# Kernel optimization log

Hardware: AMD Instinct MI355X
Metric: run time of the kernel (lower is better)

The kernel has to match this reference:

```python
import jax, jax.numpy as jnp
import numpy as np

H_IMG, W_IMG = 224, 224  # image_size default in forward


def setup_inputs() -> dict:
    key = jax.random.key(0)
    k0, k1, k2 = jax.random.split(key, 3)
    B, C, M, N = 4, 256, 1024, 16384
    xyz_feats = jax.random.normal(k0, (B, C, M), jnp.float32)
    # projections land inside the image for a realistic bin distribution
    points = jax.random.uniform(k1, (B, N, 3), jnp.float32).at[..., 2].add(0.5)
    centers = jax.random.uniform(k2, (B, M, 3), jnp.float32).at[..., 2].add(0.5)
    fx = fy = 0.5 * W_IMG  # plausible intrinsics already scaled to 224x224
    K = jnp.array([[fx, 0.0, W_IMG / 2.0],
                   [0.0, fy, H_IMG / 2.0],
                   [0.0, 0.0, 1.0]], jnp.float32)
    return {"xyz_feats": xyz_feats, "points": points, "centers": centers,
            "K": K, "kernel_size": 4}


def reference(xyz_feats, points, centers, K, kernel_size):
    B, C, M = xyz_feats.shape
    N = points.shape[1]
    H, W = H_IMG, W_IMG

    # --- interpolating_points: PointNet++ 3-NN inverse-distance interp ---
    # squared pairwise distances [B, N, M]
    d2 = (jnp.sum(points * points, -1)[:, :, None]
          + jnp.sum(centers * centers, -1)[:, None, :]
          - 2.0 * jnp.einsum('bnd,bmd->bnm', points, centers))
    neg_d, idx = jax.lax.top_k(-d2, 3)            # 3 nearest centers, [B,N,3]
    w = 1.0 / (-neg_d + 1e-8)                     # inverse-distance weights
    w = w / jnp.sum(w, -1, keepdims=True)
    b3 = jnp.arange(B)[:, None, None]
    gathered = xyz_feats[b3, :, idx]              # [B, N, 3, C]
    interp = jnp.einsum('bnkc,bnk->bnc', gathered, w)  # [B, N, C]

    # --- project_to_image ---
    uvz = jnp.einsum('ij,bnj->bni', K, points)    # [B, N, 3]
    uv = uvz[..., :2] / jnp.maximum(uvz[..., 2:], 1e-8)
    u = jnp.clip(jnp.floor(uv[..., 0]), 0, W - 1).astype(jnp.int32)
    v = jnp.clip(jnp.floor(uv[..., 1]), 0, H - 1).astype(jnp.int32)
    idx_flat = u + v * W                          # [B, N]

    # --- scatter-add binning + count normalize ---
    bb = jnp.arange(B)[:, None]
    feat_map = jnp.zeros((B, H * W, C), interp.dtype).at[bb, idx_flat].add(interp)
    count = jnp.zeros((B, H * W), interp.dtype).at[bb, idx_flat].add(1.0)
    feat_map = feat_map / jnp.maximum(count, 1.0)[..., None]
    feat_map = feat_map.reshape(B, H, W, C).transpose(0, 3, 1, 2)  # [B,C,H,W]

    # --- avg_pool2d(kernel_size, stride=kernel_size) ---
    k = kernel_size
    out = feat_map.reshape(B, C, H // k, k, W // k, k).mean(axis=(3, 5))
    return out
```

## Files before the change

### kernel.cpp

```cpp
#include <hip/hip_runtime.h>
#include <hip/hip_bf16.h>

#define H_IMG 224
#define W_IMG 224
#define B_ 4
#define C_ 256
#define M_ 1024
#define N_ 16384
#define HW_ (H_IMG * W_IMG)
#define OH_ 56
#define OW_ 56
#define NBLK_ (OH_ * OW_)
#define NBINS_ (B_ * NBLK_)
#define NT_ (B_ * N_)
#define SEG_ 32
#define MAXSEG_ (NBINS_ + NT_ / SEG_)
#define KS_ 4
#define MC_ (M_ / KS_)
#define ZTOT_ (NBINS_ * C_ + B_ * HW_ + 2 * NBINS_ + 1)

__global__ __launch_bounds__(1024) void transpose_kernel(
    const float* __restrict__ xyz, float* __restrict__ XT,
    float* __restrict__ zeroRegion)
{
    __shared__ float tile[32][33];
    int b  = blockIdx.z;
    int c0 = blockIdx.x * 32;
    int m0 = blockIdx.y * 32;
    int tx = threadIdx.x, ty = threadIdx.y;
    int flat = ((blockIdx.z * gridDim.y + blockIdx.y) * gridDim.x + blockIdx.x)
               * 1024 + ty * 32 + tx;
    for (int i = flat; i < ZTOT_; i += 1024 * 1024) zeroRegion[i] = 0.0f;
    tile[ty][tx] = xyz[(b * C_ + c0 + ty) * M_ + m0 + tx];
    __syncthreads();
    XT[(b * M_ + m0 + ty) * C_ + c0 + tx] = tile[tx][ty];
}

__global__ __launch_bounds__(1024) void top3_kernel(
    const float* __restrict__ points, const float* __restrict__ centers,
    const float* __restrict__ Kmat,
    int* __restrict__ pixA, int* __restrict__ idA, float* __restrict__ wA,
    float* __restrict__ cnt, int* __restrict__ binCnt)
{
#pragma clang fp contract(off)
    __shared__ float4 cen[M_];
    __shared__ float  pd[KS_][256][3];
    __shared__ int    pi[KS_][256][3];
    int b = blockIdx.y;
    int t = threadIdx.x;
    int p = t & 255;
    int s = t >> 8;
    int n = blockIdx.x * 256 + p;

    {
        float cx = centers[(b * M_ + t) * 3 + 0];
        float cy = centers[(b * M_ + t) * 3 + 1];
        float cz = centers[(b * M_ + t) * 3 + 2];
        float c2 = ((cx * cx) + (cy * cy)) + (cz * cz);
        cen[t] = make_float4(cx, cy, cz, c2);
    }
    __syncthreads();

    float px = points[(b * N_ + n) * 3 + 0];
    float py = points[(b * N_ + n) * 3 + 1];
    float pz = points[(b * N_ + n) * 3 + 2];
    float p2 = ((px * px) + (py * py)) + (pz * pz);

    float d0 = 1e30f, d1 = 1e30f, d2v = 1e30f;
    int   i0 = 0, i1 = 0, i2 = 0;
    int mbase = s * MC_;
#pragma unroll 4
    for (int j = 0; j < MC_; ++j) {
        int m = mbase + j;
        float4 cc = cen[m];
        float dot = ((pz * cc.z) + (py * cc.y)) + (px * cc.x);
        float d   = (p2 + cc.w) - (2.0f * dot);
        if (d < d2v) {
            if (d < d1) {
                d2v = d1; i2 = i1;
                if (d < d0) { d1 = d0; i1 = i0; d0 = d; i0 = m; }
                else        { d1 = d;  i1 = m; }
            } else { d2v = d; i2 = m; }
        }
    }
    pd[s][p][0] = d0;  pd[s][p][1] = d1;  pd[s][p][2] = d2v;
    pi[s][p][0] = i0;  pi[s][p][1] = i1;  pi[s][p][2] = i2;
    __syncthreads();

    if (t < 256) {
        float md0 = 1e30f, md1 = 1e30f, md2 = 1e30f;
        int   mi0 = M_,    mi1 = M_,    mi2 = M_;
#pragma unroll
        for (int ss = 0; ss < KS_; ++ss)
#pragma unroll
            for (int j = 0; j < 3; ++j) {
                float dd = pd[ss][t][j];
                int   ii = pi[ss][t][j];
                if ((dd < md2) || (dd == md2 && ii < mi2)) {
                    if ((dd < md1) || (dd == md1 && ii < mi1)) {
                        md2 = md1; mi2 = mi1;
                        if ((dd < md0) || (dd == md0 && ii < mi0)) {
                            md1 = md0; mi1 = mi0; md0 = dd; mi0 = ii;
                        } else { md1 = dd; mi1 = ii; }
                    } else { md2 = dd; mi2 = ii; }
                }
            }

        float w0 = 1.0f / (md0 + 1e-8f);
        float w1 = 1.0f / (md1 + 1e-8f);
        float w2 = 1.0f / (md2 + 1e-8f);
        float ws = (w0 + w1) + w2;
        w0 /= ws; w1 /= ws; w2 /= ws;

        float fx = Kmat[0], cxk = Kmat[2], fy = Kmat[4], cyk = Kmat[5];
        float u_num = (cxk * pz) + (fx * px);
        float v_num = (cyk * pz) + (fy * py);
        float zc    = fmaxf(pz, 1e-8f);
        float u = floorf(u_num / zc);
        float v = floorf(v_num / zc);
        int ui = (int)fminf(fmaxf(u, 0.0f), (float)(W_IMG - 1));
        int vi = (int)fminf(fmaxf(v, 0.0f), (float)(H_IMG - 1));
        int pix = vi * W_IMG + ui;

        int g = b * N_ + n;
        pixA[g] = pix;
        idA[g]           = mi0; idA[g + NT_]     = mi1; idA[g + 2 * NT_] = mi2;
        wA [g]           = w0;  wA [g + NT_]     = w1;  wA [g + 2 * NT_] = w2;
        atomicAdd(&cnt[b * HW_ + pix], 1.0f);
        int bin = b * NBLK_ + (vi >> 2) * OW_ + (ui >> 2);
        atomicAdd(&binCnt[bin], 1);
    }
}

__global__ __launch_bounds__(1024) void scan_kernel(
    const int* __restrict__ binCnt, int* __restrict__ binOff)
{
    const int PER = (NBINS_ + 1023) / 1024;
    __shared__ int partial[1024];
    int t = threadIdx.x;
    int base = t * PER;
    int local[PER];
    int s = 0;
#pragma unroll
    for (int j = 0; j < PER; ++j) {
        int idx = base + j;
        int v = (idx < NBINS_) ? binCnt[idx] : 0;
        local[j] = s;
        s += v;
    }
    partial[t] = s;
    __syncthreads();
    for (int ofs = 1; ofs < 1024; ofs <<= 1) {
        int v = (t >= ofs) ? partial[t - ofs] : 0;
        __syncthreads();
        partial[t] += v;
        __syncthreads();
    }
    int excl = (t == 0) ? 0 : partial[t - 1];
#pragma unroll
    for (int j = 0; j < PER; ++j) {
        int idx = base + j;
        if (idx < NBINS_) binOff[idx] = excl + local[j];
    }
}

__global__ __launch_bounds__(256) void segbuild_kernel(
    const int* __restrict__ binCnt, const int* __restrict__ binOff,
    int* __restrict__ segCounter, int4* __restrict__ segs)
{
    int bin = blockIdx.x * 256 + threadIdx.x;
    if (bin >= NBINS_) return;
    int k = binCnt[bin];
    int nseg = (k + SEG_ - 1) / SEG_;
    if (nseg == 0) nseg = 1;
    int base = atomicAdd(segCounter, nseg);
    int off = binOff[bin];
    for (int s = 0; s < nseg; ++s) {
        int len = k - s * SEG_;
        len = (len < 0) ? 0 : ((len > SEG_) ? SEG_ : len);
        segs[base + s] = make_int4(bin, off + s * SEG_, len, nseg);
    }
}

__global__ __launch_bounds__(256) void pack_kernel(
    const int* __restrict__ pixA, const int* __restrict__ idA,
    const float* __restrict__ wA, const float* __restrict__ cnt,
    const int* __restrict__ binOff, int* __restrict__ binFill,
    int4* __restrict__ idP, float4* __restrict__ wP)
{
    int g = blockIdx.x * 256 + threadIdx.x;
    int b = g >> 14;
    int pix = pixA[g];
    int u = pix % W_IMG, v = pix / W_IMG;
    int bin = b * NBLK_ + (v >> 2) * OW_ + (u >> 2);
    int pos = atomicAdd(&binFill[bin], 1);
    int dst = binOff[bin] + pos;
    float s = 0.0625f / fmaxf(cnt[b * HW_ + pix], 1.0f);
    idP[dst] = make_int4(idA[g], idA[g + NT_], idA[g + 2 * NT_], b);
    wP[dst]  = make_float4(wA[g] * s, wA[g + NT_] * s, wA[g + 2 * NT_] * s, 0.0f);
}

__global__ __launch_bounds__(256) void gather_kernel(
    const float* __restrict__ XT, const int4* __restrict__ segs,
    const int* __restrict__ segCounter, const int4* __restrict__ idP,
    const float4* __restrict__ wP, float* __restrict__ tmp)
{
    int sid = blockIdx.x;
    if (sid >= segCounter[0]) return;
    int4 sg   = segs[sid];
    int bin   = sg.x, start = sg.y, len = sg.z, nseg = sg.w;
    int b     = bin / NBLK_;
    int c     = threadIdx.x;

    __shared__ int4   sId[SEG_];
    __shared__ float4 sW [SEG_];
    if (c < len) { sId[c] = idP[start + c]; sW[c] = wP[start + c]; }
    __syncthreads();

    const float* XTb = XT + (size_t)b * (M_ * C_);
    float acc = 0.0f;
    for (int j = 0; j < len; ++j) {
        int4   id = sId[j];
        float4 w  = sW[j];
        acc = fmaf(w.x, XTb[id.x * C_ + c],
              fmaf(w.y, XTb[id.y * C_ + c],
              fmaf(w.z, XTb[id.z * C_ + c], acc)));
    }

    float* dst = &tmp[(size_t)bin * C_ + c];
    if (nseg == 1) *dst = acc;
    else           atomicAdd(dst, acc);
}

__global__ __launch_bounds__(1024) void untranspose_kernel(
    const float* __restrict__ tmp, float* __restrict__ out)
{
    __shared__ float tile[32][33];
    int b  = blockIdx.z;
    int n0 = blockIdx.x * 32;
    int c0 = blockIdx.y * 32;
    int tx = threadIdx.x, ty = threadIdx.y;
    tile[ty][tx] = tmp[((size_t)b * NBLK_ + n0 + ty) * C_ + c0 + tx];
    __syncthreads();
    out[((size_t)(b * C_ + c0 + ty)) * NBLK_ + n0 + tx] = tile[tx][ty];
}

extern "C" void kernel_launch(void* const* d_in, const int* in_sizes, int n_in,
                              void* d_out, int out_size, void* d_ws, size_t ws_size,
                              hipStream_t stream)
{
    const float* xyz_feats = (const float*)d_in[0];
    const float* points    = (const float*)d_in[1];
    const float* centers   = (const float*)d_in[2];
    const float* Kmat      = (const float*)d_in[3];

    float* out = (float*)d_out;

    float*  XT       = (float*)d_ws;
    int4*   idP      = (int4*)(XT + (size_t)B_ * M_ * C_);
    float4* wP       = (float4*)(idP + NT_);
    int4*   segs     = (int4*)(wP + NT_);
    float*  tmp      = (float*)(segs + MAXSEG_);
    float*  cnt      = tmp + (size_t)NBINS_ * C_;
    int*    binCnt   = (int*)(cnt + (size_t)B_ * HW_);
    int*    binFill  = binCnt + NBINS_;
    int*    segCounter = binFill + NBINS_;
    int*    pixA     = segCounter + 1;
    int*    idA      = pixA + NT_;
    float*  wA       = (float*)(idA + 3 * NT_);
    int*    binOff   = (int*)(wA + 3 * NT_);

    dim3 tb(32, 32);
    dim3 tg(C_ / 32, M_ / 32, B_);
    transpose_kernel<<<tg, tb, 0, stream>>>(xyz_feats, XT, tmp);

    dim3 bg(N_ / 256, B_);
    top3_kernel<<<bg, 1024, 0, stream>>>(points, centers, Kmat,
                                         pixA, idA, wA, cnt, binCnt);

    scan_kernel<<<1, 1024, 0, stream>>>(binCnt, binOff);

    segbuild_kernel<<<(NBINS_ + 255) / 256, 256, 0, stream>>>(
        binCnt, binOff, segCounter, segs);

    pack_kernel<<<NT_ / 256, 256, 0, stream>>>(pixA, idA, wA, cnt,
                                               binOff, binFill, idP, wP);

    gather_kernel<<<MAXSEG_, 256, 0, stream>>>(XT, segs, segCounter,
                                               idP, wP, tmp);

    dim3 ug(NBLK_ / 32, C_ / 32, B_);
    untranspose_kernel<<<ug, tb, 0, stream>>>(tmp, out);
}
```

Measured before the change: 178.0 us.

## Register-block two points per thread in top3 and fuse segment build into scan

The top-3 search now gives each thread two query points and splits the centers into 8 slices instead of 4, so each shared-memory center load is reused for two distance computations. The segment-building kernel is folded into the single-block scan by also scanning per-bin segment counts, which removes one launch and the global atomic counter. The cost is higher register pressure in top3, a larger shared reduction buffer, and serial segment writes inside the single scan block.

```diff
diff --git a/kernel.cpp b/kernel.cpp
--- a/kernel.cpp
+++ b/kernel.cpp
@@ -15,7 +15,7 @@
 #define NT_ (B_ * N_)
 #define SEG_ 32
 #define MAXSEG_ (NBINS_ + NT_ / SEG_)
-#define KS_ 4
+#define KS_ 8
 #define MC_ (M_ / KS_)
 #define ZTOT_ (NBINS_ * C_ + B_ * HW_ + 2 * NBINS_ + 1)
 
@@ -46,11 +46,11 @@
     __shared__ float4 cen[M_];
     __shared__ float  pd[KS_][256][3];
     __shared__ int    pi[KS_][256][3];
-    int b = blockIdx.y;
-    int t = threadIdx.x;
-    int p = t & 255;
-    int s = t >> 8;
-    int n = blockIdx.x * 256 + p;
+    int b  = blockIdx.y;
+    int t  = threadIdx.x;
+    int pl = t & 127;
+    int s  = t >> 7;
+    int nbase = blockIdx.x * 256;
 
     {
         float cx = centers[(b * M_ + t) * 3 + 0];
@@ -61,30 +61,45 @@
     }
     __syncthreads();
 
-    float px = points[(b * N_ + n) * 3 + 0];
-    float py = points[(b * N_ + n) * 3 + 1];
-    float pz = points[(b * N_ + n) * 3 + 2];
-    float p2 = ((px * px) + (py * py)) + (pz * pz);
-
-    float d0 = 1e30f, d1 = 1e30f, d2v = 1e30f;
-    int   i0 = 0, i1 = 0, i2 = 0;
+    int nA = b * N_ + nbase + pl;
+    int nB = nA + 128;
+    float pxA = points[nA * 3 + 0], pyA = points[nA * 3 + 1], pzA = points[nA * 3 + 2];
+    float pxB = points[nB * 3 + 0], pyB = points[nB * 3 + 1], pzB = points[nB * 3 + 2];
+    float p2A = ((pxA * pxA) + (pyA * pyA)) + (pzA * pzA);
+    float p2B = ((pxB * pxB) + (pyB * pyB)) + (pzB * pzB);
+
+    float d0a = 1e30f, d1a = 1e30f, d2a = 1e30f;
+    int   i0a = 0, i1a = 0, i2a = 0;
+    float d0b = 1e30f, d1b = 1e30f, d2b = 1e30f;
+    int   i0b = 0, i1b = 0, i2b = 0;
     int mbase = s * MC_;
-#pragma unroll 4
+#pragma unroll 2
     for (int j = 0; j < MC_; ++j) {
         int m = mbase + j;
         float4 cc = cen[m];
-        float dot = ((pz * cc.z) + (py * cc.y)) + (px * cc.x);
-        float d   = (p2 + cc.w) - (2.0f * dot);
-        if (d < d2v) {
-            if (d < d1) {
-                d2v = d1; i2 = i1;
-                if (d < d0) { d1 = d0; i1 = i0; d0 = d; i0 = m; }
-                else        { d1 = d;  i1 = m; }
-            } else { d2v = d; i2 = m; }
+        float dotA = ((pzA * cc.z) + (pyA * cc.y)) + (pxA * cc.x);
+        float dA   = (p2A + cc.w) - (2.0f * dotA);
+        float dotB = ((pzB * cc.z) + (pyB * cc.y)) + (pxB * cc.x);
+        float dB   = (p2B + cc.w) - (2.0f * dotB);
+        if (dA < d2a) {
+            if (dA < d1a) {
+                d2a = d1a; i2a = i1a;
+                if (dA < d0a) { d1a = d0a; i1a = i0a; d0a = dA; i0a = m; }
+                else          { d1a = dA;  i1a = m; }
+            } else { d2a = dA; i2a = m; }
         }
-    }
-    pd[s][p][0] = d0;  pd[s][p][1] = d1;  pd[s][p][2] = d2v;
-    pi[s][p][0] = i0;  pi[s][p][1] = i1;  pi[s][p][2] = i2;
+        if (dB < d2b) {
+            if (dB < d1b) {
+                d2b = d1b; i2b = i1b;
+                if (dB < d0b) { d1b = d0b; i1b = i0b; d0b = dB; i0b = m; }
+                else          { d1b = dB;  i1b = m; }
+            } else { d2b = dB; i2b = m; }
+        }
+    }
+    pd[s][pl][0] = d0a;  pd[s][pl][1] = d1a;  pd[s][pl][2] = d2a;
+    pi[s][pl][0] = i0a;  pi[s][pl][1] = i1a;  pi[s][pl][2] = i2a;
+    pd[s][pl + 128][0] = d0b;  pd[s][pl + 128][1] = d1b;  pd[s][pl + 128][2] = d2b;
+    pi[s][pl + 128][0] = i0b;  pi[s][pl + 128][1] = i1b;  pi[s][pl + 128][2] = i2b;
     __syncthreads();
 
     if (t < 256) {
@@ -112,6 +127,10 @@
         float ws = (w0 + w1) + w2;
         w0 /= ws; w1 /= ws; w2 /= ws;
 
+        int n = nbase + t;
+        int g = b * N_ + n;
+        float px = points[g * 3 + 0], py = points[g * 3 + 1], pz = points[g * 3 + 2];
+
         float fx = Kmat[0], cxk = Kmat[2], fy = Kmat[4], cyk = Kmat[5];
         float u_num = (cxk * pz) + (fx * px);
         float v_num = (cyk * pz) + (fy * py);
@@ -122,7 +141,6 @@
         int vi = (int)fminf(fmaxf(v, 0.0f), (float)(H_IMG - 1));
         int pix = vi * W_IMG + ui;
 
-        int g = b * N_ + n;
         pixA[g] = pix;
         idA[g]           = mi0; idA[g + NT_]     = mi1; idA[g + 2 * NT_] = mi2;
         wA [g]           = w0;  wA [g + NT_]     = w1;  wA [g + 2 * NT_] = w2;
@@ -133,53 +151,51 @@
 }
 
 __global__ __launch_bounds__(1024) void scan_kernel(
-    const int* __restrict__ binCnt, int* __restrict__ binOff)
+    const int* __restrict__ binCnt, int* __restrict__ binOff,
+    int4* __restrict__ segs, int* __restrict__ segTotal)
 {
     const int PER = (NBINS_ + 1023) / 1024;
-    __shared__ int partial[1024];
+    __shared__ int partK[1024], partS[1024];
     int t = threadIdx.x;
     int base = t * PER;
-    int local[PER];
-    int s = 0;
+    int localK[PER], localS[PER];
+    int sk = 0, sn = 0;
 #pragma unroll
     for (int j = 0; j < PER; ++j) {
         int idx = base + j;
-        int v = (idx < NBINS_) ? binCnt[idx] : 0;
-        local[j] = s;
-        s += v;
-    }
-    partial[t] = s;
+        int k  = (idx < NBINS_) ? binCnt[idx] : 0;
+        int ns = 0;
+        if (idx < NBINS_) { ns = (k + SEG_ - 1) / SEG_; if (ns == 0) ns = 1; }
+        localK[j] = sk; localS[j] = sn;
+        sk += k; sn += ns;
+    }
+    partK[t] = sk; partS[t] = sn;
     __syncthreads();
     for (int ofs = 1; ofs < 1024; ofs <<= 1) {
-        int v = (t >= ofs) ? partial[t - ofs] : 0;
+        int vK = (t >= ofs) ? partK[t - ofs] : 0;
+        int vS = (t >= ofs) ? partS[t - ofs] : 0;
         __syncthreads();
-        partial[t] += v;
+        partK[t] += vK; partS[t] += vS;
         __syncthreads();
     }
-    int excl = (t == 0) ? 0 : partial[t - 1];
+    int exK = (t == 0) ? 0 : partK[t - 1];
+    int exS = (t == 0) ? 0 : partS[t - 1];
 #pragma unroll
     for (int j = 0; j < PER; ++j) {
         int idx = base + j;
-        if (idx < NBINS_) binOff[idx] = excl + local[j];
-    }
-}
-
-__global__ __launch_bounds__(256) void segbuild_kernel(
-    const int* __restrict__ binCnt, const int* __restrict__ binOff,
-    int* __restrict__ segCounter, int4* __restrict__ segs)
-{
-    int bin = blockIdx.x * 256 + threadIdx.x;
-    if (bin >= NBINS_) return;
-    int k = binCnt[bin];
-    int nseg = (k + SEG_ - 1) / SEG_;
-    if (nseg == 0) nseg = 1;
-    int base = atomicAdd(segCounter, nseg);
-    int off = binOff[bin];
-    for (int s = 0; s < nseg; ++s) {
-        int len = k - s * SEG_;
-        len = (len < 0) ? 0 : ((len > SEG_) ? SEG_ : len);
-        segs[base + s] = make_int4(bin, off + s * SEG_, len, nseg);
-    }
+        if (idx >= NBINS_) continue;
+        int off = exK + localK[j];
+        int sb  = exS + localS[j];
+        binOff[idx] = off;
+        int k = binCnt[idx];
+        int nseg = (k + SEG_ - 1) / SEG_; if (nseg == 0) nseg = 1;
+        for (int q = 0; q < nseg; ++q) {
+            int len = k - q * SEG_;
+            len = (len < 0) ? 0 : ((len > SEG_) ? SEG_ : len);
+            segs[sb + q] = make_int4(idx, off + q * SEG_, len, nseg);
+        }
+    }
+    if (t == 0) segTotal[0] = partS[1023];
 }
 
 __global__ __launch_bounds__(256) void pack_kernel(
@@ -202,11 +218,11 @@
 
 __global__ __launch_bounds__(256) void gather_kernel(
     const float* __restrict__ XT, const int4* __restrict__ segs,
-    const int* __restrict__ segCounter, const int4* __restrict__ idP,
+    const int* __restrict__ segTotal, const int4* __restrict__ idP,
     const float4* __restrict__ wP, float* __restrict__ tmp)
 {
     int sid = blockIdx.x;
-    if (sid >= segCounter[0]) return;
+    if (sid >= segTotal[0]) return;
     int4 sg   = segs[sid];
     int bin   = sg.x, start = sg.y, len = sg.z, nseg = sg.w;
     int b     = bin / NBLK_;
@@ -264,8 +280,8 @@
     float*  cnt      = tmp + (size_t)NBINS_ * C_;
     int*    binCnt   = (int*)(cnt + (size_t)B_ * HW_);
     int*    binFill  = binCnt + NBINS_;
-    int*    segCounter = binFill + NBINS_;
-    int*    pixA     = segCounter + 1;
+    int*    segTotal = binFill + NBINS_;
+    int*    pixA     = segTotal + 1;
     int*    idA      = pixA + NT_;
     float*  wA       = (float*)(idA + 3 * NT_);
     int*    binOff   = (int*)(wA + 3 * NT_);
@@ -278,15 +294,12 @@
     top3_kernel<<<bg, 1024, 0, stream>>>(points, centers, Kmat,
                                          pixA, idA, wA, cnt, binCnt);
 
-    scan_kernel<<<1, 1024, 0, stream>>>(binCnt, binOff);
-
-    segbuild_kernel<<<(NBINS_ + 255) / 256, 256, 0, stream>>>(
-        binCnt, binOff, segCounter, segs);
+    scan_kernel<<<1, 1024, 0, stream>>>(binCnt, binOff, segs, segTotal);
 
     pack_kernel<<<NT_ / 256, 256, 0, stream>>>(pixA, idA, wA, cnt,
                                                binOff, binFill, idP, wP);
 
-    gather_kernel<<<MAXSEG_, 256, 0, stream>>>(XT, segs, segCounter,
+    gather_kernel<<<MAXSEG_, 256, 0, stream>>>(XT, segs, segTotal,
                                                idP, wP, tmp);
 
     dim3 ug(NBLK_ / 32, C_ / 32, B_);
```

New measurement: 187.5 us. +5.4%, slower.
